# Optimization experiments

Measured on AMD Instinct MI355X. Metric: run time of the kernel, lower is better.

The kernel has to match this reference:

```python
import jax, jax.numpy as jnp
import numpy as np

EPS = 1e-8
ALPHA = 1.0


def setup_inputs() -> dict:
    key = jax.random.key(0)
    k1, k2 = jax.random.split(key)
    N = 8192
    pred = jax.random.normal(k1, (N,), dtype=jnp.float32)
    gt = jax.random.normal(k2, (N,), dtype=jnp.float32)
    return {"pred": pred, "gt": gt, "n": N}


def _rank_counts(x):
    # sa[i] = #{j : x[i] > x[j]}  (pairwise O(N^2) comparison, reduced per row)
    return jnp.sum((x[:, None] > x[None, :]).astype(x.dtype), axis=-1)


def reference(pred, gt, n):
    N = pred.shape[0]
    sa = _rank_counts(pred)                 # [N]
    sb = _rank_counts(gt)                   # [N]
    delta = (sa - sb) / (N + EPS)           # rank disagreement, normalized
    a2 = jax.lax.stop_gradient(pred) - delta * ALPHA  # pred.detach() - delta*alpha
    l = jnp.abs(pred - a2)                  # L1, reduction='none'
    return jnp.sum(l) / n
```

## Files before the change

kernel.cpp:

```cpp
#include <hip/hip_runtime.h>


constexpr int T    = 1024;
constexpr int NI   = 32;
constexpr int NN   = 8192;
constexpr int JW   = NN / NI;
constexpr int PAD  = 32;
constexpr unsigned BIAS = 0x40000000u;

__global__ __launch_bounds__(T) void score_loss_one(
    const float* __restrict__ pred,
    const float* __restrict__ gt,
    unsigned* __restrict__ bsum,
    float* __restrict__ out,
    double inv)
{
    __shared__ float sp[NN];
    __shared__ float sg[NN];
    __shared__ int dsum[NI];
    __shared__ unsigned wred[16];

    const int tid = threadIdx.x;
    const int b   = blockIdx.x;
    const int il  = tid & 31;
    const int s   = tid >> 5;
    const int i   = b * NI + il;

    const float xi = pred[i];
    const float yi = gt[i];

    if (tid < NI) dsum[tid] = 0;

    {
        const float4* ps = reinterpret_cast<const float4*>(pred);
        const float4* gs = reinterpret_cast<const float4*>(gt);
        float4* spd = reinterpret_cast<float4*>(sp);
        float4* sgd = reinterpret_cast<float4*>(sg);
#pragma unroll
        for (int k = 0; k < (NN / 4) / T; ++k) {
            spd[k * T + tid] = ps[k * T + tid];
            sgd[k * T + tid] = gs[k * T + tid];
        }
    }
    __syncthreads();

    int d = 0;
    {
        const float4* wp = reinterpret_cast<const float4*>(sp + s * JW);
        const float4* wg = reinterpret_cast<const float4*>(sg + s * JW);
#pragma unroll 8
        for (int t = 0; t < JW / 4; ++t) {
            float4 p = wp[t];
            float4 g = wg[t];
            d += (xi > p.x) + (xi > p.y) + (xi > p.z) + (xi > p.w);
            d -= (yi > g.x) + (yi > g.y) + (yi > g.z) + (yi > g.w);
        }
    }

    d += __shfl_xor(d, 32, 64);
    if ((tid & 63) < 32) atomicAdd(&dsum[il], d);
    __syncthreads();

    if (tid < NI) {
        int v = dsum[tid];
        v = (v < 0) ? -v : v;
#pragma unroll
        for (int off = 16; off >= 1; off >>= 1)
            v += __shfl_xor(v, off, 64);
        if (tid == 0)
            __hip_atomic_store(&bsum[b * PAD], (unsigned)v + BIAS,
                               __ATOMIC_RELEASE, __HIP_MEMORY_SCOPE_AGENT);
    }

    if (b == 0) {
        __syncthreads();
        unsigned acc = 0;
        if (tid < 256) {
            for (;;) {
                unsigned v = __hip_atomic_load(&bsum[tid * PAD],
                                               __ATOMIC_RELAXED,
                                               __HIP_MEMORY_SCOPE_AGENT);
                unsigned diff = v - BIAS;
                if (diff <= 262144u) { acc = diff; break; }
                __builtin_amdgcn_s_sleep(8);
            }
        }
        for (int off = 1; off < 64; off <<= 1)
            acc += __shfl_xor(acc, off, 64);
        if ((tid & 63) == 0) wred[tid >> 6] = acc;
        __syncthreads();
        if (tid == 0) {
            unsigned tot = 0;
#pragma unroll
            for (int w = 0; w < 16; ++w) tot += wred[w];
            out[0] = (float)((double)tot * inv);
        }
    }
}

extern "C" void kernel_launch(void* const* d_in, const int* in_sizes, int n_in,
                              void* d_out, int out_size, void* d_ws, size_t ws_size,
                              hipStream_t stream)
{
    const float* pred = (const float*)d_in[0];
    const float* gt   = (const float*)d_in[1];
    const int N = in_sizes[0];

    float* out     = (float*)d_out;
    unsigned* bsum = (unsigned*)d_ws;

    const double inv = 1.0 / (((double)N + 1e-8) * (double)N);

    dim3 grid(N / NI);
    score_loss_one<<<grid, T, 0, stream>>>(pred, gt, bsum, out, inv);
}
```

Baseline: 17.49 us.

## Register-block four rows per thread to cut LDS reads in rank comparison

Each thread now holds four pred/gt row values in registers and compares them against a shared j-slice. This reuses every shared-memory float4 load across four rows instead of one. The block shrinks to 512 threads and the j-range is split into 64 segments. Partial counts are then reduced with a wider xor-shuffle tree before the atomic adds into shared memory. In exchange, each thread carries more registers and has a longer serial loop, and the block has fewer waves to hide latency.

```diff
diff --git a/kernel.cpp b/kernel.cpp
--- a/kernel.cpp
+++ b/kernel.cpp
@@ -1,10 +1,11 @@
 #include <hip/hip_runtime.h>
 
 
-constexpr int T    = 1024;
+constexpr int T    = 512;
 constexpr int NI   = 32;
 constexpr int NN   = 8192;
-constexpr int JW   = NN / NI;
+constexpr int NW   = 64;
+constexpr int JW   = NN / NW;
 constexpr int PAD  = 32;
 constexpr unsigned BIAS = 0x40000000u;
 
@@ -18,16 +19,17 @@
     __shared__ float sp[NN];
     __shared__ float sg[NN];
     __shared__ int dsum[NI];
-    __shared__ unsigned wred[16];
+    __shared__ unsigned wred[T / 64];
 
     const int tid = threadIdx.x;
     const int b   = blockIdx.x;
-    const int il  = tid & 31;
-    const int s   = tid >> 5;
-    const int i   = b * NI + il;
+    const int il4 = tid & 7;
+    const int s   = tid >> 3;
+    const int ib  = b * NI + il4 * 4;
 
-    const float xi = pred[i];
-    const float yi = gt[i];
+    float xi[4], yi[4];
+#pragma unroll
+    for (int c = 0; c < 4; ++c) { xi[c] = pred[ib + c]; yi[c] = gt[ib + c]; }
 
     if (tid < NI) dsum[tid] = 0;
 
@@ -44,21 +46,33 @@
     }
     __syncthreads();
 
-    int d = 0;
+    int d[4] = {0, 0, 0, 0};
     {
         const float4* wp = reinterpret_cast<const float4*>(sp + s * JW);
         const float4* wg = reinterpret_cast<const float4*>(sg + s * JW);
-#pragma unroll 8
+#pragma unroll 4
         for (int t = 0; t < JW / 4; ++t) {
             float4 p = wp[t];
             float4 g = wg[t];
-            d += (xi > p.x) + (xi > p.y) + (xi > p.z) + (xi > p.w);
-            d -= (yi > g.x) + (yi > g.y) + (yi > g.z) + (yi > g.w);
+#pragma unroll
+            for (int c = 0; c < 4; ++c) {
+                d[c] += (xi[c] > p.x) + (xi[c] > p.y) + (xi[c] > p.z) + (xi[c] > p.w);
+                d[c] -= (yi[c] > g.x) + (yi[c] > g.y) + (yi[c] > g.z) + (yi[c] > g.w);
+            }
         }
     }
 
-    d += __shfl_xor(d, 32, 64);
-    if ((tid & 63) < 32) atomicAdd(&dsum[il], d);
+#pragma unroll
+    for (int c = 0; c < 4; ++c) {
+#pragma unroll
+        for (int off = 8; off < 64; off <<= 1)
+            d[c] += __shfl_xor(d[c], off, 64);
+    }
+    if ((tid & 63) < 8) {
+#pragma unroll
+        for (int c = 0; c < 4; ++c)
+            atomicAdd(&dsum[il4 * 4 + c], d[c]);
+    }
     __syncthreads();
 
     if (tid < NI) {
@@ -92,7 +106,7 @@
         if (tid == 0) {
             unsigned tot = 0;
 #pragma unroll
-            for (int w = 0; w < 16; ++w) tot += wred[w];
+            for (int w = 0; w < T / 64; ++w) tot += wred[w];
             out[0] = (float)((double)tot * inv);
         }
     }
```

Result: slower. 18.58 us (+6.2%).
